# Performance work log

Hardware: AMD Instinct MI355X
Metric: run time of the kernel (lower is better)

The kernel has to match this reference:

```python
import jax, jax.numpy as jnp
import numpy as np

D_MODEL = 768
N_HEADS = 12
D_FFN = 3072
BATCH = 16
SEQ = 1024


def _layer_norm(x, g, b, eps=1e-5):
    mu = jnp.mean(x, axis=-1, keepdims=True)
    var = jnp.var(x, axis=-1, keepdims=True)
    return (x - mu) * jax.lax.rsqrt(var + eps) * g + b


def setup_inputs() -> dict:
    key = jax.random.key(0)
    ks = jax.random.split(key, 8)
    s = 0.02  # init scale for weights
    return {
        "x": jax.random.normal(ks[0], (BATCH, SEQ, D_MODEL), jnp.float32),
        "ln1_g": jnp.ones((D_MODEL,), jnp.float32),
        "ln1_b": jnp.zeros((D_MODEL,), jnp.float32),
        "wq": jax.random.normal(ks[1], (D_MODEL, D_MODEL), jnp.float32) * s,
        "bq": jnp.zeros((D_MODEL,), jnp.float32),
        "wk": jax.random.normal(ks[2], (D_MODEL, D_MODEL), jnp.float32) * s,
        "bk": jnp.zeros((D_MODEL,), jnp.float32),
        "wv": jax.random.normal(ks[3], (D_MODEL, D_MODEL), jnp.float32) * s,
        "bv": jnp.zeros((D_MODEL,), jnp.float32),
        "wo": jax.random.normal(ks[4], (D_MODEL, D_MODEL), jnp.float32) * s,
        "bo": jnp.zeros((D_MODEL,), jnp.float32),
        "ln2_g": jnp.ones((D_MODEL,), jnp.float32),
        "ln2_b": jnp.zeros((D_MODEL,), jnp.float32),
        "w1": jax.random.normal(ks[5], (D_MODEL, D_FFN), jnp.float32) * s,
        "b1": jnp.zeros((D_FFN,), jnp.float32),
        "w2": jax.random.normal(ks[6], (D_FFN, D_MODEL), jnp.float32) * s,
        "b2": jnp.zeros((D_MODEL,), jnp.float32),
    }


def _block(x, ln1_g, ln1_b, wq, bq, wk, bk, wv, bv, wo, bo,
           ln2_g, ln2_b, w1, b1, w2, b2):
    bz, seq, d = x.shape
    dk = d // N_HEADS
    h = _layer_norm(x, ln1_g, ln1_b)
    q = (h @ wq + bq).reshape(bz, seq, N_HEADS, dk).transpose(0, 2, 1, 3)
    k = (h @ wk + bk).reshape(bz, seq, N_HEADS, dk).transpose(0, 2, 1, 3)
    v = (h @ wv + bv).reshape(bz, seq, N_HEADS, dk).transpose(0, 2, 1, 3)
    scores = jnp.einsum("bhqd,bhkd->bhqk", q, k) / jnp.sqrt(jnp.float32(dk))
    probs = jax.nn.softmax(scores, axis=-1)  # dropout p=0 -> identity
    attn = jnp.einsum("bhqk,bhkd->bhqd", probs, v)
    attn = attn.transpose(0, 2, 1, 3).reshape(bz, seq, d)
    x = x + attn @ wo + bo
    h = _layer_norm(x, ln2_g, ln2_b)
    # torch nn.GELU default is exact (erf) gelu
    mlp = jax.nn.gelu(h @ w1 + b1, approximate=False) @ w2 + b2
    return x + mlp


def reference(x, ln1_g, ln1_b, wq, bq, wk, bk, wv, bv, wo, bo,
              ln2_g, ln2_b, w1, b1, w2, b2):
    return _block(x, ln1_g, ln1_b, wq, bq, wk, bk, wv, bv, wo, bo,
                  ln2_g, ln2_b, w1, b1, w2, b2)
```

## Files before the change

### kernel.cpp

```cpp
#include <hip/hip_runtime.h>
#include <hip/hip_bf16.h>
#include <math.h>

typedef __bf16 bf16x8 __attribute__((ext_vector_type(8)));
typedef __bf16 bf16x4 __attribute__((ext_vector_type(4)));
typedef float f32x4 __attribute__((ext_vector_type(4)));
typedef unsigned int u32x2 __attribute__((ext_vector_type(2)));

__device__ __forceinline__ f32x4 mfma16(bf16x8 a, bf16x8 b, f32x4 c) {
  return __builtin_amdgcn_mfma_f32_16x16x32_bf16(a, b, c, 0, 0, 0);
}

__device__ __forceinline__ float gelu_f(float v) {
  float x2 = v * v;
  float u = v * __builtin_fmaf(0.044715f, x2, 1.0f);
  float z = __builtin_amdgcn_exp2f(2.302101862f * u);
  float r = __builtin_amdgcn_rcpf(z + 1.0f);
  return __builtin_fmaf(-v, r, v);
}

__device__ __forceinline__ void async16(const void* g, void* l) {
  __builtin_amdgcn_global_load_lds((const __attribute__((address_space(1))) unsigned int*)g,
                                   (__attribute__((address_space(3))) unsigned int*)l, 16, 0, 0);
}

__device__ __forceinline__ unsigned lds_off(const void* p) {
  return (unsigned)(unsigned long long)(const __attribute__((address_space(3))) void*)p;
}

__global__ __launch_bounds__(256) void wprep_kernel(const float* __restrict__ W, __bf16* __restrict__ Wt,
                                                    int K, int N) {
  __shared__ __bf16 tile[64][65];
  const int tn0 = blockIdx.x * 64, tk0 = blockIdx.y * 64;
  const int tr = threadIdx.x >> 4, tc = (threadIdx.x & 15) * 4;
#pragma unroll
  for (int p = 0; p < 4; ++p) {
    int r = p * 16 + tr;
    float4 v = *(const float4*)&W[(long)(tk0 + r) * N + tn0 + tc];
    tile[tc + 0][r] = (__bf16)v.x;
    tile[tc + 1][r] = (__bf16)v.y;
    tile[tc + 2][r] = (__bf16)v.z;
    tile[tc + 3][r] = (__bf16)v.w;
  }
  __syncthreads();
#pragma unroll
  for (int p = 0; p < 4; ++p) {
    int n = p * 16 + tr;
    bf16x4 o;
    o[0] = tile[n][tc]; o[1] = tile[n][tc + 1]; o[2] = tile[n][tc + 2]; o[3] = tile[n][tc + 3];
    *(bf16x4*)&Wt[(long)(tn0 + n) * K + tk0 + tc] = o;
  }
}

__global__ void bias_cat_kernel(const float* __restrict__ bq, const float* __restrict__ bk,
                                const float* __restrict__ bv, float* __restrict__ o) {
  int i = blockIdx.x * 256 + threadIdx.x;
  if (i >= 2304) return;
  o[i] = (i < 768) ? bq[i] : (i < 1536) ? bk[i - 768] : bv[i - 1536];
}

__global__ __launch_bounds__(256) void ln_kernel(const float* __restrict__ x, const float* __restrict__ g,
                                                 const float* __restrict__ b, __bf16* __restrict__ out) {
  int row = blockIdx.x;
  const float* xr = x + (long)row * 768;
  float v0 = xr[threadIdx.x], v1 = xr[threadIdx.x + 256], v2 = xr[threadIdx.x + 512];
  float s = v0 + v1 + v2, s2 = v0 * v0 + v1 * v1 + v2 * v2;
#pragma unroll
  for (int m = 1; m < 64; m <<= 1) { s += __shfl_xor(s, m); s2 += __shfl_xor(s2, m); }
  __shared__ float ws1[4], ws2[4];
  int wv = threadIdx.x >> 6;
  if ((threadIdx.x & 63) == 0) { ws1[wv] = s; ws2[wv] = s2; }
  __syncthreads();
  s = ws1[0] + ws1[1] + ws1[2] + ws1[3];
  s2 = ws2[0] + ws2[1] + ws2[2] + ws2[3];
  float mu = s * (1.0f / 768.0f);
  float var = s2 * (1.0f / 768.0f) - mu * mu;
  float rstd = rsqrtf(var + 1e-5f);
  __bf16* orow = out + (long)row * 768;
  orow[threadIdx.x]       = (__bf16)((v0 - mu) * rstd * g[threadIdx.x]       + b[threadIdx.x]);
  orow[threadIdx.x + 256] = (__bf16)((v1 - mu) * rstd * g[threadIdx.x + 256] + b[threadIdx.x + 256]);
  orow[threadIdx.x + 512] = (__bf16)((v2 - mu) * rstd * g[threadIdx.x + 512] + b[threadIdx.x + 512]);
}

__global__ __launch_bounds__(256) void ln_b_kernel(const __bf16* __restrict__ x, const float* __restrict__ g,
                                                   const float* __restrict__ b, __bf16* __restrict__ out) {
  int row = blockIdx.x;
  const __bf16* xr = x + (long)row * 768;
  float v0 = (float)xr[threadIdx.x], v1 = (float)xr[threadIdx.x + 256], v2 = (float)xr[threadIdx.x + 512];
  float s = v0 + v1 + v2, s2 = v0 * v0 + v1 * v1 + v2 * v2;
#pragma unroll
  for (int m = 1; m < 64; m <<= 1) { s += __shfl_xor(s, m); s2 += __shfl_xor(s2, m); }
  __shared__ float ws1[4], ws2[4];
  int wv = threadIdx.x >> 6;
  if ((threadIdx.x & 63) == 0) { ws1[wv] = s; ws2[wv] = s2; }
  __syncthreads();
  s = ws1[0] + ws1[1] + ws1[2] + ws1[3];
  s2 = ws2[0] + ws2[1] + ws2[2] + ws2[3];
  float mu = s * (1.0f / 768.0f);
  float var = s2 * (1.0f / 768.0f) - mu * mu;
  float rstd = rsqrtf(var + 1e-5f);
  __bf16* orow = out + (long)row * 768;
  orow[threadIdx.x]       = (__bf16)((v0 - mu) * rstd * g[threadIdx.x]       + b[threadIdx.x]);
  orow[threadIdx.x + 256] = (__bf16)((v1 - mu) * rstd * g[threadIdx.x + 256] + b[threadIdx.x + 256]);
  orow[threadIdx.x + 512] = (__bf16)((v2 - mu) * rstd * g[threadIdx.x + 512] + b[threadIdx.x + 512]);
}

template <int EPI>
__global__ __launch_bounds__(256, 3) void gemm_kernel(const __bf16* __restrict__ A, const __bf16* __restrict__ Wt,
                                                      const float* __restrict__ bias, const float* __restrict__ resf,
                                                      const __bf16* __restrict__ resb,
                                                      float* __restrict__ outf, __bf16* __restrict__ outb,
                                                      int M, int N, int K) {
  __shared__ __align__(16) __bf16 As[8192];
  __shared__ __align__(16) __bf16 Bs[8192];
  const int tid = threadIdx.x, lane = tid & 63, w = tid >> 6;
  const int wm = w >> 1, wn = w & 1, lr = lane & 15, lh = lane >> 4;
  const int gx = gridDim.x, gy = gridDim.y;
  int id = blockIdx.x + gx * blockIdx.y;
  int xcd = id & 7, slot = id >> 3;
  int by = xcd * (gy >> 3) + slot / gx;
  int bx = slot % gx;
  const int m0 = by * 128, n0 = bx * 128;
  const int nt = K >> 6;
  int srow[4], scol[4];
#pragma unroll
  for (int l = 0; l < 4; ++l) {
    int c = l * 256 + tid;
    srow[l] = c >> 3;
    scol[l] = ((c & 7) ^ ((c >> 3) & 7)) * 8;
  }
  const __bf16* Ag = A + (long)m0 * K;
  const __bf16* Bg = Wt + (long)n0 * K;

  f32x4 acc[4][4] = {};
  for (int t = 0; t < nt; ++t) {
    const int kb = t << 6;
    __syncthreads();
#pragma unroll
    for (int l = 0; l < 4; ++l) {
      async16(Ag + (long)srow[l] * K + kb + scol[l], &As[l * 2048 + w * 512]);
      async16(Bg + (long)srow[l] * K + kb + scol[l], &Bs[l * 2048 + w * 512]);
    }
    __syncthreads();
    bf16x8 af[4][2], bfr[4][2];
#pragma unroll
    for (int m4 = 0; m4 < 4; ++m4) {
      int row = wm * 64 + m4 * 16 + lr;
#pragma unroll
      for (int kk = 0; kk < 2; ++kk)
        af[m4][kk] = *(const bf16x8*)&As[row * 64 + ((kk * 32 + lh * 8) ^ ((row & 7) << 3))];
    }
#pragma unroll
    for (int n = 0; n < 4; ++n) {
      int row = wn * 64 + n * 16 + lr;
#pragma unroll
      for (int kk = 0; kk < 2; ++kk)
        bfr[n][kk] = *(const bf16x8*)&Bs[row * 64 + ((kk * 32 + lh * 8) ^ ((row & 7) << 3))];
    }
    __builtin_amdgcn_s_setprio(1);
#pragma unroll
    for (int m4 = 0; m4 < 4; ++m4)
#pragma unroll
      for (int n = 0; n < 4; ++n) {
        acc[m4][n] = mfma16(af[m4][0], bfr[n][0], acc[m4][n]);
        acc[m4][n] = mfma16(af[m4][1], bfr[n][1], acc[m4][n]);
      }
    __builtin_amdgcn_s_setprio(0);
  }

#pragma unroll
  for (int m = 0; m < 4; ++m)
#pragma unroll
    for (int n = 0; n < 4; ++n) {
      int col = n0 + wn * 64 + n * 16 + lr;
      float bc = bias[col];
#pragma unroll
      for (int j = 0; j < 4; ++j) {
        int row = m0 + wm * 64 + m * 16 + lh * 4 + j;
        float v = acc[m][n][j] + bc;
        if (EPI == 1) v = gelu_f(v);
        if (EPI == 3) outb[(long)row * N + col] = (__bf16)(v + resf[(long)row * N + col]);
        else if (EPI == 4) outf[(long)row * N + col] = v + (float)resb[(long)row * N + col];
        else outb[(long)row * N + col] = (__bf16)v;
      }
    }
}

__global__ __launch_bounds__(256) void attn_kernel(const __bf16* __restrict__ qkv, __bf16* __restrict__ o) {
  __shared__ __bf16 K_lds[64][72];
  __shared__ __align__(16) unsigned char Vt[8448];
  __shared__ __align__(16) unsigned char Pt[4][4224];
  const int tid = threadIdx.x;
  const int lane = tid & 63, wv = tid >> 6;
  const int lr = lane & 15, lh = lane >> 4;
  const int hb = blockIdx.x, qt = blockIdx.y;
  const int h = hb % 12, bz = hb / 12;
  const int qrow0 = bz * 1024 + qt * 128 + wv * 32;
  const int hcol = h * 64;
  const __bf16* q = qkv + hcol;
  const __bf16* k = qkv + 768 + hcol;
  const __bf16* v = qkv + 1536 + hcol;
  const float QSC = 0.18033688011112042f;
  bf16x8 aq[2][2];
#pragma unroll
  for (int r = 0; r < 2; ++r)
#pragma unroll
    for (int kk = 0; kk < 2; ++kk) {
      bf16x8 t = *(const bf16x8*)(q + (long)(qrow0 + r * 16 + lr) * 2304 + kk * 32 + lh * 8);
#pragma unroll
      for (int e = 0; e < 8; ++e) t[e] = (__bf16)((float)t[e] * QSC);
      aq[r][kk] = t;
    }
  bf16x8 ones;
#pragma unroll
  for (int e = 0; e < 8; ++e) ones[e] = (__bf16)1.0f;
  f32x4 o_fr[2][4] = {};
  float l_s[2][4];
#pragma unroll
  for (int r = 0; r < 2; ++r)
#pragma unroll
    for (int j = 0; j < 4; ++j) l_s[r][j] = 0.0f;
  const int r0 = tid >> 3, c0 = (tid & 7) * 8;
  const unsigned vt0 = lds_off(Vt) + (lane >> 4) * 1056 + (lane & 15) * 2;
  const int Tst = (r0 >> 2) * 4 + (c0 >> 4);
  const int vb = Tst * 128 + (r0 & 3) * 32 + (c0 & 15) * 2 + (Tst >> 3) * 32;
  const unsigned pwb = lds_off(&Pt[wv][0]) + (lr >> 2) * 256 + (lr & 3) * 32 + lh * 8;
  const unsigned prb = lds_off(&Pt[wv][0]) + lh * 512 + (lh >> 1) * 32 + lr * 2;

  bf16x8 rK[2], rV[2];
#pragma unroll
  for (int p = 0; p < 2; ++p) {
    long gr = (long)(bz * 1024 + p * 32 + r0) * 2304 + c0;
    rK[p] = *(const bf16x8*)(k + gr);
    rV[p] = *(const bf16x8*)(v + gr);
  }
#pragma unroll
  for (int p = 0; p < 2; ++p) {
    *(bf16x8*)&K_lds[p * 32 + r0][c0] = rK[p];
    *(bf16x8*)(Vt + vb + p * 4224) = rV[p];
  }
  __syncthreads();

  for (int t = 0; t < 16; ++t) {
    bf16x8 bk[4][2];
#pragma unroll
    for (int n = 0; n < 4; ++n)
#pragma unroll
      for (int kk = 0; kk < 2; ++kk)
        bk[n][kk] = *(const bf16x8*)&K_lds[n * 16 + lr][kk * 32 + lh * 8];
    if (t < 15) {
#pragma unroll
      for (int p = 0; p < 2; ++p) {
        long gr = (long)(bz * 1024 + (t + 1) * 64 + p * 32 + r0) * 2304 + c0;
        rK[p] = *(const bf16x8*)(k + gr);
        rV[p] = *(const bf16x8*)(v + gr);
      }
    }
    f32x4 sf[2][4];
    __builtin_amdgcn_s_setprio(1);
#pragma unroll
    for (int r = 0; r < 2; ++r)
#pragma unroll
      for (int n = 0; n < 4; ++n) {
        f32x4 s = {0.f, 0.f, 0.f, 0.f};
        s = mfma16(aq[r][0], bk[n][0], s);
        s = mfma16(aq[r][1], bk[n][1], s);
        sf[r][n] = s;
      }
    __builtin_amdgcn_s_setprio(0);
#define PW(rr, nn)                                                                     \
    {                                                                                  \
      float e0 = __builtin_amdgcn_exp2f(sf[rr][nn][0]);                                \
      float e1 = __builtin_amdgcn_exp2f(sf[rr][nn][1]);                                \
      float e2 = __builtin_amdgcn_exp2f(sf[rr][nn][2]);                                \
      float e3 = __builtin_amdgcn_exp2f(sf[rr][nn][3]);                                \
      u32x2 d;                                                                         \
      asm("v_cvt_pk_bf16_f32 %0, %1, %2" : "=v"(d[0]) : "v"(e0), "v"(e1));             \
      asm("v_cvt_pk_bf16_f32 %0, %1, %2" : "=v"(d[1]) : "v"(e2), "v"(e3));             \
      asm volatile("ds_write_b64 %0, %1 offset:%2" ::"v"(pwb), "v"(d),                 \
                   "i"((nn)*1056 + (rr)*128) : "memory");                              \
    }
    PW(0, 0) PW(0, 1) PW(0, 2) PW(0, 3) PW(1, 0) PW(1, 1) PW(1, 2) PW(1, 3)
#undef PW
    asm volatile("s_waitcnt lgkmcnt(0)" ::: "memory");
    __builtin_amdgcn_sched_barrier(0);
    u32x2 trv[4][2][2];
#pragma unroll
    for (int d0 = 0; d0 < 4; ++d0)
#pragma unroll
      for (int ks = 0; ks < 2; ++ks) {
        unsigned a = vt0 + ks * 4224 + d0 * 128;
        asm volatile("ds_read_b64_tr_b16 %0, %1" : "=v"(trv[d0][ks][0]) : "v"(a));
        asm volatile("ds_read_b64_tr_b16 %0, %1 offset:512" : "=v"(trv[d0][ks][1]) : "v"(a));
      }
    u32x2 trp[2][2][2];
#define PR(rr, kks)                                                                     \
    asm volatile("ds_read_b64_tr_b16 %0, %1 offset:%2"                                  \
                 : "=v"(trp[rr][kks][0]) : "v"(prb), "i"((rr)*128 + (kks)*2112));       \
    asm volatile("ds_read_b64_tr_b16 %0, %1 offset:%2"                                  \
                 : "=v"(trp[rr][kks][1]) : "v"(prb), "i"((rr)*128 + (kks)*2112 + 256));
    PR(0, 0) PR(0, 1) PR(1, 0) PR(1, 1)
#undef PR
    asm volatile("s_waitcnt lgkmcnt(0)" ::: "memory");
    __builtin_amdgcn_sched_barrier(0);
    __syncthreads();
    if (t < 15) {
#pragma unroll
      for (int p = 0; p < 2; ++p) {
        *(bf16x8*)&K_lds[p * 32 + r0][c0] = rK[p];
        *(bf16x8*)(Vt + vb + p * 4224) = rV[p];
      }
    }
    bf16x8 ap[2][2];
#pragma unroll
    for (int r = 0; r < 2; ++r)
#pragma unroll
      for (int ks = 0; ks < 2; ++ks) {
        union { u32x2 u[2]; bf16x8 v8; } pu;
        pu.u[0] = trp[r][ks][0];
        pu.u[1] = trp[r][ks][1];
        ap[r][ks] = pu.v8;
      }
    __builtin_amdgcn_s_setprio(1);
#pragma unroll
    for (int r = 0; r < 2; ++r) {
      f32x4 ls = {0.f, 0.f, 0.f, 0.f};
      ls = mfma16(ap[r][0], ones, ls);
      ls = mfma16(ap[r][1], ones, ls);
#pragma unroll
      for (int j = 0; j < 4; ++j) l_s[r][j] += ls[j];
    }
#pragma unroll
    for (int d0 = 0; d0 < 4; ++d0) {
      union { u32x2 u[2]; bf16x8 v8; } b0, b1;
      b0.u[0] = trv[d0][0][0]; b0.u[1] = trv[d0][0][1];
      b1.u[0] = trv[d0][1][0]; b1.u[1] = trv[d0][1][1];
#pragma unroll
      for (int r = 0; r < 2; ++r) {
        o_fr[r][d0] = mfma16(ap[r][0], b0.v8, o_fr[r][d0]);
        o_fr[r][d0] = mfma16(ap[r][1], b1.v8, o_fr[r][d0]);
      }
    }
    __builtin_amdgcn_s_setprio(0);
    if (t < 15) __syncthreads();
  }
#pragma unroll
  for (int r = 0; r < 2; ++r)
#pragma unroll
    for (int d = 0; d < 4; ++d)
#pragma unroll
      for (int j = 0; j < 4; ++j) {
        int row = qrow0 + r * 16 + lh * 4 + j;
        int col = hcol + d * 16 + lr;
        o[(long)row * 768 + col] = (__bf16)(o_fr[r][d][j] * (1.0f / l_s[r][j]));
      }
}

extern "C" void kernel_launch(void* const* d_in, const int* in_sizes, int n_in,
                              void* d_out, int out_size, void* d_ws, size_t ws_size,
                              hipStream_t stream) {
  const float* x    = (const float*)d_in[0];
  const float* ln1g = (const float*)d_in[1];
  const float* ln1b = (const float*)d_in[2];
  const float* wq   = (const float*)d_in[3];
  const float* bq   = (const float*)d_in[4];
  const float* wk   = (const float*)d_in[5];
  const float* bk   = (const float*)d_in[6];
  const float* wv   = (const float*)d_in[7];
  const float* bv   = (const float*)d_in[8];
  const float* wo   = (const float*)d_in[9];
  const float* bo   = (const float*)d_in[10];
  const float* ln2g = (const float*)d_in[11];
  const float* ln2b = (const float*)d_in[12];
  const float* w1   = (const float*)d_in[13];
  const float* b1   = (const float*)d_in[14];
  const float* w2   = (const float*)d_in[15];
  const float* b2   = (const float*)d_in[16];
  float* out = (float*)d_out;
  char* ws = (char*)d_ws;

  const long SD = 16384L * 768;
  const long SF = 16384L * 3072;

  __bf16* qkv = (__bf16*)(ws);
  __bf16* f1  = (__bf16*)(ws);
  __bf16* hb  = (__bf16*)(ws + 2 * SF);
  __bf16* x2  = (__bf16*)(ws + 2 * SF + 2 * SD);
  __bf16* h2  = (__bf16*)(ws + 2 * SF + 2 * SD + 4 * SD);
  __bf16* wtqkv = (__bf16*)(ws + 2 * SF + 2 * SD + 4 * SD + 2 * SD);
  __bf16* wto = wtqkv + 2304L * 768;
  __bf16* wt1 = wto + 768L * 768;
  __bf16* wt2 = wt1 + 768L * 3072;
  float*  bqkv = (float*)(wt2 + 3072L * 768);

  wprep_kernel<<<dim3(12, 12), 256, 0, stream>>>(wq, wtqkv,               768, 768);
  wprep_kernel<<<dim3(12, 12), 256, 0, stream>>>(wk, wtqkv + 768L * 768,  768, 768);
  wprep_kernel<<<dim3(12, 12), 256, 0, stream>>>(wv, wtqkv + 1536L * 768, 768, 768);
  wprep_kernel<<<dim3(12, 12), 256, 0, stream>>>(wo, wto, 768, 768);
  wprep_kernel<<<dim3(48, 12), 256, 0, stream>>>(w1, wt1, 768, 3072);
  wprep_kernel<<<dim3(12, 48), 256, 0, stream>>>(w2, wt2, 3072, 768);
  bias_cat_kernel<<<9, 256, 0, stream>>>(bq, bk, bv, bqkv);

  ln_kernel<<<16384, 256, 0, stream>>>(x, ln1g, ln1b, hb);
  gemm_kernel<0><<<dim3(18, 128), 256, 0, stream>>>(hb, wtqkv, bqkv, nullptr, nullptr, nullptr, qkv, 16384, 2304, 768);
  attn_kernel<<<dim3(192, 8), 256, 0, stream>>>(qkv, hb);
  gemm_kernel<3><<<dim3(6, 128), 256, 0, stream>>>(hb, wto, bo, x, nullptr, nullptr, x2, 16384, 768, 768);
  ln_b_kernel<<<16384, 256, 0, stream>>>(x2, ln2g, ln2b, h2);
  gemm_kernel<1><<<dim3(24, 128), 256, 0, stream>>>(h2, wt1, b1, nullptr, nullptr, nullptr, f1, 16384, 3072, 768);
  gemm_kernel<4><<<dim3(6, 128), 256, 0, stream>>>(f1, wt2, b2, nullptr, x2, out, nullptr, 16384, 768, 3072);
}
```

Measured before the change: 378.2 us.

## Double-buffer K/V tiles in attention LDS and drop a per-iteration barrier

```diff
diff --git a/kernel.cpp b/kernel.cpp
--- a/kernel.cpp
+++ b/kernel.cpp
@@ -187,8 +187,8 @@
 }
 
 __global__ __launch_bounds__(256) void attn_kernel(const __bf16* __restrict__ qkv, __bf16* __restrict__ o) {
-  __shared__ __bf16 K_lds[64][72];
-  __shared__ __align__(16) unsigned char Vt[8448];
+  __shared__ __bf16 K_lds[2][64][72];
+  __shared__ __align__(16) unsigned char Vt[2][8448];
   __shared__ __align__(16) unsigned char Pt[4][4224];
   const int tid = threadIdx.x;
   const int lane = tid & 63, wv = tid >> 6;
@@ -221,39 +221,44 @@
 #pragma unroll
     for (int j = 0; j < 4; ++j) l_s[r][j] = 0.0f;
   const int r0 = tid >> 3, c0 = (tid & 7) * 8;
-  const unsigned vt0 = lds_off(Vt) + (lane >> 4) * 1056 + (lane & 15) * 2;
+  const unsigned vt0 = lds_off(&Vt[0][0]) + (lane >> 4) * 1056 + (lane & 15) * 2;
   const int Tst = (r0 >> 2) * 4 + (c0 >> 4);
   const int vb = Tst * 128 + (r0 & 3) * 32 + (c0 & 15) * 2 + (Tst >> 3) * 32;
   const unsigned pwb = lds_off(&Pt[wv][0]) + (lr >> 2) * 256 + (lr & 3) * 32 + lh * 8;
   const unsigned prb = lds_off(&Pt[wv][0]) + lh * 512 + (lh >> 1) * 32 + lr * 2;
 
-  bf16x8 rK[2], rV[2];
+  const __bf16* kp[2];
+  const __bf16* vp[2];
 #pragma unroll
   for (int p = 0; p < 2; ++p) {
     long gr = (long)(bz * 1024 + p * 32 + r0) * 2304 + c0;
-    rK[p] = *(const bf16x8*)(k + gr);
-    rV[p] = *(const bf16x8*)(v + gr);
-  }
+    kp[p] = k + gr;
+    vp[p] = v + gr;
+  }
+  bf16x8 rK[2], rV[2];
+#pragma unroll
+  for (int p = 0; p < 2; ++p) { rK[p] = *(const bf16x8*)kp[p]; rV[p] = *(const bf16x8*)vp[p]; }
 #pragma unroll
   for (int p = 0; p < 2; ++p) {
-    *(bf16x8*)&K_lds[p * 32 + r0][c0] = rK[p];
-    *(bf16x8*)(Vt + vb + p * 4224) = rV[p];
+    *(bf16x8*)&K_lds[0][p * 32 + r0][c0] = rK[p];
+    *(bf16x8*)(&Vt[0][0] + vb + p * 4224) = rV[p];
   }
   __syncthreads();
 
   for (int t = 0; t < 16; ++t) {
+    const int cur = t & 1, nxt = cur ^ 1;
     bf16x8 bk[4][2];
 #pragma unroll
     for (int n = 0; n < 4; ++n)
 #pragma unroll
       for (int kk = 0; kk < 2; ++kk)
-        bk[n][kk] = *(const bf16x8*)&K_lds[n * 16 + lr][kk * 32 + lh * 8];
+        bk[n][kk] = *(const bf16x8*)&K_lds[cur][n * 16 + lr][kk * 32 + lh * 8];
     if (t < 15) {
 #pragma unroll
       for (int p = 0; p < 2; ++p) {
-        long gr = (long)(bz * 1024 + (t + 1) * 64 + p * 32 + r0) * 2304 + c0;
-        rK[p] = *(const bf16x8*)(k + gr);
-        rV[p] = *(const bf16x8*)(v + gr);
+        kp[p] += 64 * 2304; vp[p] += 64 * 2304;
+        rK[p] = *(const bf16x8*)kp[p];
+        rV[p] = *(const bf16x8*)vp[p];
       }
     }
     f32x4 sf[2][4];
@@ -282,17 +287,20 @@
     }
     PW(0, 0) PW(0, 1) PW(0, 2) PW(0, 3) PW(1, 0) PW(1, 1) PW(1, 2) PW(1, 3)
 #undef PW
-    asm volatile("s_waitcnt lgkmcnt(0)" ::: "memory");
+    u32x2 trv[4][2][2];
+    {
+      unsigned vtc = vt0 + (unsigned)cur * 8448u;
+#pragma unroll
+      for (int d0 = 0; d0 < 4; ++d0)
+#pragma unroll
+        for (int ks = 0; ks < 2; ++ks) {
+          unsigned a = vtc + ks * 4224 + d0 * 128;
+          asm volatile("ds_read_b64_tr_b16 %0, %1" : "=v"(trv[d0][ks][0]) : "v"(a));
+          asm volatile("ds_read_b64_tr_b16 %0, %1 offset:512" : "=v"(trv[d0][ks][1]) : "v"(a));
+        }
+    }
+    asm volatile("s_waitcnt lgkmcnt(15)" ::: "memory");
     __builtin_amdgcn_sched_barrier(0);
-    u32x2 trv[4][2][2];
-#pragma unroll
-    for (int d0 = 0; d0 < 4; ++d0)
-#pragma unroll
-      for (int ks = 0; ks < 2; ++ks) {
-        unsigned a = vt0 + ks * 4224 + d0 * 128;
-        asm volatile("ds_read_b64_tr_b16 %0, %1" : "=v"(trv[d0][ks][0]) : "v"(a));
-        asm volatile("ds_read_b64_tr_b16 %0, %1 offset:512" : "=v"(trv[d0][ks][1]) : "v"(a));
-      }
     u32x2 trp[2][2][2];
 #define PR(rr, kks)                                                                     \
     asm volatile("ds_read_b64_tr_b16 %0, %1 offset:%2"                                  \
@@ -303,12 +311,11 @@
 #undef PR
     asm volatile("s_waitcnt lgkmcnt(0)" ::: "memory");
     __builtin_amdgcn_sched_barrier(0);
-    __syncthreads();
     if (t < 15) {
 #pragma unroll
       for (int p = 0; p < 2; ++p) {
-        *(bf16x8*)&K_lds[p * 32 + r0][c0] = rK[p];
-        *(bf16x8*)(Vt + vb + p * 4224) = rV[p];
+        *(bf16x8*)&K_lds[nxt][p * 32 + r0][c0] = rK[p];
+        *(bf16x8*)(&Vt[nxt][0] + vb + p * 4224) = rV[p];
       }
     }
     bf16x8 ap[2][2];
```

Result: no change. 381.6 us (+0.9%).

## Widen attention blocks to 8 waves sharing each K/V tile, relax LDS wait

Applied to the files above, without the earlier changes.

```diff
diff --git a/kernel.cpp b/kernel.cpp
--- a/kernel.cpp
+++ b/kernel.cpp
@@ -186,16 +186,16 @@
     }
 }
 
-__global__ __launch_bounds__(256) void attn_kernel(const __bf16* __restrict__ qkv, __bf16* __restrict__ o) {
+__global__ __launch_bounds__(512) void attn_kernel(const __bf16* __restrict__ qkv, __bf16* __restrict__ o) {
   __shared__ __bf16 K_lds[64][72];
   __shared__ __align__(16) unsigned char Vt[8448];
-  __shared__ __align__(16) unsigned char Pt[4][4224];
+  __shared__ __align__(16) unsigned char Pt[8][4224];
   const int tid = threadIdx.x;
   const int lane = tid & 63, wv = tid >> 6;
   const int lr = lane & 15, lh = lane >> 4;
   const int hb = blockIdx.x, qt = blockIdx.y;
   const int h = hb % 12, bz = hb / 12;
-  const int qrow0 = bz * 1024 + qt * 128 + wv * 32;
+  const int qrow0 = bz * 1024 + qt * 256 + wv * 32;
   const int hcol = h * 64;
   const __bf16* q = qkv + hcol;
   const __bf16* k = qkv + 768 + hcol;
@@ -227,18 +227,12 @@
   const unsigned pwb = lds_off(&Pt[wv][0]) + (lr >> 2) * 256 + (lr & 3) * 32 + lh * 8;
   const unsigned prb = lds_off(&Pt[wv][0]) + lh * 512 + (lh >> 1) * 32 + lr * 2;
 
-  bf16x8 rK[2], rV[2];
-#pragma unroll
-  for (int p = 0; p < 2; ++p) {
-    long gr = (long)(bz * 1024 + p * 32 + r0) * 2304 + c0;
-    rK[p] = *(const bf16x8*)(k + gr);
-    rV[p] = *(const bf16x8*)(v + gr);
-  }
-#pragma unroll
-  for (int p = 0; p < 2; ++p) {
-    *(bf16x8*)&K_lds[p * 32 + r0][c0] = rK[p];
-    *(bf16x8*)(Vt + vb + p * 4224) = rV[p];
-  }
+  const __bf16* kp = k + (long)(bz * 1024 + r0) * 2304 + c0;
+  const __bf16* vp = v + (long)(bz * 1024 + r0) * 2304 + c0;
+  bf16x8 rK = *(const bf16x8*)kp;
+  bf16x8 rV = *(const bf16x8*)vp;
+  *(bf16x8*)&K_lds[r0][c0] = rK;
+  *(bf16x8*)(Vt + vb) = rV;
   __syncthreads();
 
   for (int t = 0; t < 16; ++t) {
@@ -249,12 +243,9 @@
       for (int kk = 0; kk < 2; ++kk)
         bk[n][kk] = *(const bf16x8*)&K_lds[n * 16 + lr][kk * 32 + lh * 8];
     if (t < 15) {
-#pragma unroll
-      for (int p = 0; p < 2; ++p) {
-        long gr = (long)(bz * 1024 + (t + 1) * 64 + p * 32 + r0) * 2304 + c0;
-        rK[p] = *(const bf16x8*)(k + gr);
-        rV[p] = *(const bf16x8*)(v + gr);
-      }
+      kp += 64 * 2304; vp += 64 * 2304;
+      rK = *(const bf16x8*)kp;
+      rV = *(const bf16x8*)vp;
     }
     f32x4 sf[2][4];
     __builtin_amdgcn_s_setprio(1);
@@ -282,8 +273,6 @@
     }
     PW(0, 0) PW(0, 1) PW(0, 2) PW(0, 3) PW(1, 0) PW(1, 1) PW(1, 2) PW(1, 3)
 #undef PW
-    asm volatile("s_waitcnt lgkmcnt(0)" ::: "memory");
-    __builtin_amdgcn_sched_barrier(0);
     u32x2 trv[4][2][2];
 #pragma unroll
     for (int d0 = 0; d0 < 4; ++d0)
@@ -293,6 +282,8 @@
         asm volatile("ds_read_b64_tr_b16 %0, %1" : "=v"(trv[d0][ks][0]) : "v"(a));
         asm volatile("ds_read_b64_tr_b16 %0, %1 offset:512" : "=v"(trv[d0][ks][1]) : "v"(a));
       }
+    asm volatile("s_waitcnt lgkmcnt(15)" ::: "memory");
+    __builtin_amdgcn_sched_barrier(0);
     u32x2 trp[2][2][2];
 #define PR(rr, kks)                                                                     \
     asm volatile("ds_read_b64_tr_b16 %0, %1 offset:%2"                                  \
@@ -305,11 +296,8 @@
     __builtin_amdgcn_sched_barrier(0);
     __syncthreads();
     if (t < 15) {
-#pragma unroll
-      for (int p = 0; p < 2; ++p) {
-        *(bf16x8*)&K_lds[p * 32 + r0][c0] = rK[p];
-        *(bf16x8*)(Vt + vb + p * 4224) = rV[p];
-      }
+      *(bf16x8*)&K_lds[r0][c0] = rK;
+      *(bf16x8*)(Vt + vb) = rV;
     }
     bf16x8 ap[2][2];
 #pragma unroll
@@ -403,7 +391,7 @@
 
   ln_kernel<<<16384, 256, 0, stream>>>(x, ln1g, ln1b, hb);
   gemm_kernel<0><<<dim3(18, 128), 256, 0, stream>>>(hb, wtqkv, bqkv, nullptr, nullptr, nullptr, qkv, 16384, 2304, 768);
-  attn_kernel<<<dim3(192, 8), 256, 0, stream>>>(qkv, hb);
+  attn_kernel<<<dim3(192, 4), 512, 0, stream>>>(qkv, hb);
   gemm_kernel<3><<<dim3(6, 128), 256, 0, stream>>>(hb, wto, bo, x, nullptr, nullptr, x2, 16384, 768, 768);
   ln_b_kernel<<<16384, 256, 0, stream>>>(x2, ln2g, ln2b, h2);
   gemm_kernel<1><<<dim3(24, 128), 256, 0, stream>>>(h2, wt1, b1, nullptr, nullptr, nullptr, f1, 16384, 3072, 768);
```

Result: faster. 370.2 us (-2.1%).
